# Kernel tuning notes

Hardware: AMD Instinct MI355X
Metric: run time of the kernel (lower is better)

## Reference

```python
import jax, jax.numpy as jnp
import numpy as np

B, T, D, H, O = 64, 2048, 64, 512, 128


def setup_inputs() -> dict:
    key = jax.random.key(0)
    ks = jax.random.split(key, 7)
    s = 1.0 / np.sqrt(H).astype(np.float32)  # PyTorch default uniform(-1/sqrt(H), 1/sqrt(H))
    u = lambda k, shp: jax.random.uniform(k, shp, jnp.float32, -s, s)
    return {
        "x": jax.random.normal(ks[0], (B, T, D), jnp.float32),
        "W_ih": u(ks[1], (4 * H, D)),
        "W_hh": u(ks[2], (4 * H, H)),
        "b_ih": u(ks[3], (4 * H,)),
        "b_hh": u(ks[4], (4 * H,)),
        "W_out": u(ks[5], (O, H)),
        "b_out": u(ks[6], (O,)),
        "batch_size": B,
    }


def reference(x, W_ih, W_hh, b_ih, b_hh, W_out, b_out, batch_size):
    Bv, Tv, Dv = x.shape
    Hv = W_hh.shape[1]
    # Precompute input-to-gate projections for all timesteps: [T, B, 4H]
    xg = (jnp.einsum("btd,gd->btg", x, W_ih) + b_ih + b_hh).transpose(1, 0, 2)
    h0 = jnp.zeros((Bv, Hv), x.dtype)
    c0 = jnp.zeros((Bv, Hv), x.dtype)

    def step(carry, g_t):
        h, c = carry
        g = g_t + h @ W_hh.T  # [B, 4H]
        i, f, gc, o = jnp.split(g, 4, axis=-1)  # PyTorch gate order i,f,g,o
        i = jax.nn.sigmoid(i)
        f = jax.nn.sigmoid(f)
        gc = jnp.tanh(gc)
        o = jax.nn.sigmoid(o)
        c = f * c + i * gc
        h = o * jnp.tanh(c)
        return (h, c), None

    (hT, cT), _ = jax.lax.scan(step, (h0, c0), xg)
    # Linear applied at last timestep only (module returns predictions[:, -1, :])
    pred = hT @ W_out.T + b_out  # [B, O]
    return pred, hT[None], cT[None]  # (pred, h_n[1,B,H], c_n[1,B,H])
```

## Files before the change

### kernel.cpp

```cpp
#include <hip/hip_runtime.h>
#include <hip/hip_bf16.h>


typedef short short8 __attribute__((ext_vector_type(8)));
typedef float floatx4 __attribute__((ext_vector_type(4)));

#define T_STEPS 2048
#define NBG 4
#define NGI 32
#define SB() __builtin_amdgcn_sched_barrier(0)

__device__ __forceinline__ unsigned short f2bf(float f){
    unsigned u = __builtin_bit_cast(unsigned, f);
    u += 0x7FFFu + ((u >> 16) & 1u);
    return (unsigned short)(u >> 16);
}

__device__ __forceinline__ short8 pack8(float4 a, float4 b){
    short8 s;
    s[0]=(short)f2bf(a.x); s[1]=(short)f2bf(a.y); s[2]=(short)f2bf(a.z); s[3]=(short)f2bf(a.w);
    s[4]=(short)f2bf(b.x); s[5]=(short)f2bf(b.y); s[6]=(short)f2bf(b.z); s[7]=(short)f2bf(b.w);
    return s;
}

__device__ __forceinline__ float fsigmoid(float x){ return 1.0f/(1.0f+__expf(-x)); }
__device__ __forceinline__ float ftanh(float x){ return 2.0f*fsigmoid(2.0f*x)-1.0f; }

__device__ __forceinline__ void xload4(float4* X, const float* base){
    asm volatile(
    "global_load_dwordx4 %0, %4, off\n\t"
    "global_load_dwordx4 %1, %4, off offset:16\n\t"
    "global_load_dwordx4 %2, %4, off offset:128\n\t"
    "global_load_dwordx4 %3, %4, off offset:144"
    : "=&v"(X[0]), "=&v"(X[1]), "=&v"(X[2]), "=&v"(X[3])
    : "v"(base) : "memory");
}

__device__ __forceinline__ void hload16_sc1(short8* A, const unsigned short* base){
    asm volatile(
    "global_load_dwordx4 %0, %16, off sc1\n\t"
    "global_load_dwordx4 %1, %16, off offset:64 sc1\n\t"
    "global_load_dwordx4 %2, %16, off offset:128 sc1\n\t"
    "global_load_dwordx4 %3, %16, off offset:192 sc1\n\t"
    "global_load_dwordx4 %4, %16, off offset:256 sc1\n\t"
    "global_load_dwordx4 %5, %16, off offset:320 sc1\n\t"
    "global_load_dwordx4 %6, %16, off offset:384 sc1\n\t"
    "global_load_dwordx4 %7, %16, off offset:448 sc1\n\t"
    "global_load_dwordx4 %8, %16, off offset:512 sc1\n\t"
    "global_load_dwordx4 %9, %16, off offset:576 sc1\n\t"
    "global_load_dwordx4 %10, %16, off offset:640 sc1\n\t"
    "global_load_dwordx4 %11, %16, off offset:704 sc1\n\t"
    "global_load_dwordx4 %12, %16, off offset:768 sc1\n\t"
    "global_load_dwordx4 %13, %16, off offset:832 sc1\n\t"
    "global_load_dwordx4 %14, %16, off offset:896 sc1\n\t"
    "global_load_dwordx4 %15, %16, off offset:960 sc1"
    : "=&v"(A[0]), "=&v"(A[1]), "=&v"(A[2]), "=&v"(A[3]),
      "=&v"(A[4]), "=&v"(A[5]), "=&v"(A[6]), "=&v"(A[7]),
      "=&v"(A[8]), "=&v"(A[9]), "=&v"(A[10]), "=&v"(A[11]),
      "=&v"(A[12]), "=&v"(A[13]), "=&v"(A[14]), "=&v"(A[15])
    : "v"(base) : "memory");
}

__global__ __launch_bounds__(64, 1)
void lstm_persist(const float* __restrict__ x,
                  const float* __restrict__ W_ih,
                  const float* __restrict__ W_hh,
                  const float* __restrict__ b_ih,
                  const float* __restrict__ b_hh,
                  const float* __restrict__ W_out,
                  const float* __restrict__ b_out,
                  float* __restrict__ out,
                  unsigned short* __restrict__ hbuf,
                  unsigned* __restrict__ flags)
{
    const int wg   = blockIdx.x;
    const int bg   = wg & 3;
    const int gi   = wg >> 2;
    const int lane = threadIdx.x;
    const int ln   = lane & 15;
    const int lk   = lane >> 4;
    const int hd0  = gi << 4;

    __shared__ __align__(16) unsigned short hl[256];

    short8 bw[4][18];
#pragma unroll
    for (int g = 0; g < 4; ++g){
        const int row = g * 512 + hd0 + ln;
        const float* pih = W_ih + row * 64 + lk * 8;
#pragma unroll
        for (int kk = 0; kk < 2; ++kk){
            float4 u0 = *reinterpret_cast<const float4*>(pih + kk * 32);
            float4 u1 = *reinterpret_cast<const float4*>(pih + kk * 32 + 4);
            bw[g][kk] = pack8(u0, u1);
        }
        const float* phh = W_hh + row * 512 + lk * 8;
#pragma unroll
        for (int kk = 2; kk < 18; ++kk){
            float4 u0 = *reinterpret_cast<const float4*>(phh + (kk - 2) * 32);
            float4 u1 = *reinterpret_cast<const float4*>(phh + (kk - 2) * 32 + 4);
            bw[g][kk] = pack8(u0, u1);
        }
    }

    float bias[4];
#pragma unroll
    for (int g = 0; g < 4; ++g){
        const int col = g * 512 + hd0 + ln;
        bias[g] = b_ih[col] + b_hh[col];
    }

    float c0 = 0.f, c1 = 0.f, c2 = 0.f, c3 = 0.f;
    const int xrow = bg * 16 + ln;

    const unsigned* fpoll = flags + bg * NGI + (lane & 31);
    unsigned* fme = flags + bg * NGI + gi;

    short8 a[18];
    float4 xr[4];
    xload4(xr, x + ((size_t)xrow * T_STEPS) * 64 + lk * 8);

    for (int t = 0; t < T_STEPS; ++t){
        if (t > 0){
            unsigned fv;
            do {
                asm volatile("global_load_dword %0, %1, off sc1\n\t"
                             "s_waitcnt vmcnt(0)"
                             : "=v"(fv) : "v"(fpoll) : "memory");
            } while (!__all((int)(fv >= (unsigned)t)));
            SB();
            const unsigned short* hp =
                hbuf + (size_t)((((t & 1) ^ 1) * NBG + bg) * 16 + ln) * 512 + lk * 8;
            hload16_sc1(&a[2], hp);
        } else {
            asm volatile("s_waitcnt vmcnt(0)" ::: "memory");
            SB();
        }

        a[0] = pack8(xr[0], xr[1]);
        a[1] = pack8(xr[2], xr[3]);

        floatx4 acc0 = {bias[0], bias[0], bias[0], bias[0]};
        floatx4 acc1 = {bias[1], bias[1], bias[1], bias[1]};
        floatx4 acc2 = {bias[2], bias[2], bias[2], bias[2]};
        floatx4 acc3 = {bias[3], bias[3], bias[3], bias[3]};
#pragma unroll
        for (int kk = 0; kk < 2; ++kk){
            acc0 = __builtin_amdgcn_mfma_f32_16x16x32_bf16(a[kk], bw[0][kk], acc0, 0, 0, 0);
            acc1 = __builtin_amdgcn_mfma_f32_16x16x32_bf16(a[kk], bw[1][kk], acc1, 0, 0, 0);
            acc2 = __builtin_amdgcn_mfma_f32_16x16x32_bf16(a[kk], bw[2][kk], acc2, 0, 0, 0);
            acc3 = __builtin_amdgcn_mfma_f32_16x16x32_bf16(a[kk], bw[3][kk], acc3, 0, 0, 0);
        }

        if (t > 0){
            asm volatile("s_waitcnt vmcnt(8)" ::: "memory");
            SB();
#pragma unroll
            for (int kk = 2; kk < 10; ++kk){
                acc0 = __builtin_amdgcn_mfma_f32_16x16x32_bf16(a[kk], bw[0][kk], acc0, 0, 0, 0);
                acc1 = __builtin_amdgcn_mfma_f32_16x16x32_bf16(a[kk], bw[1][kk], acc1, 0, 0, 0);
                acc2 = __builtin_amdgcn_mfma_f32_16x16x32_bf16(a[kk], bw[2][kk], acc2, 0, 0, 0);
                acc3 = __builtin_amdgcn_mfma_f32_16x16x32_bf16(a[kk], bw[3][kk], acc3, 0, 0, 0);
            }
            asm volatile("s_waitcnt vmcnt(0)" ::: "memory");
            SB();
#pragma unroll
            for (int kk = 10; kk < 18; ++kk){
                acc0 = __builtin_amdgcn_mfma_f32_16x16x32_bf16(a[kk], bw[0][kk], acc0, 0, 0, 0);
                acc1 = __builtin_amdgcn_mfma_f32_16x16x32_bf16(a[kk], bw[1][kk], acc1, 0, 0, 0);
                acc2 = __builtin_amdgcn_mfma_f32_16x16x32_bf16(a[kk], bw[2][kk], acc2, 0, 0, 0);
                acc3 = __builtin_amdgcn_mfma_f32_16x16x32_bf16(a[kk], bw[3][kk], acc3, 0, 0, 0);
            }
        }

#define EPI(R, CREG)                                                         \
        {   float iv = fsigmoid(acc0[R]);                                    \
            float fv_ = fsigmoid(acc1[R]);                                   \
            float gv = ftanh(acc2[R]);                                       \
            float ov = fsigmoid(acc3[R]);                                    \
            CREG = fv_ * CREG + iv * gv;                                     \
            float hv = ov * ftanh(CREG);                                     \
            hl[(lk * 4 + R) * 16 + ln] = f2bf(hv);                           \
            if (t == T_STEPS - 1){                                           \
                int rr = bg * 16 + lk * 4 + R;                               \
                out[8192  + rr * 512 + hd0 + ln] = hv;                       \
                out[40960 + rr * 512 + hd0 + ln] = CREG;                     \
            }                                                                \
        }
        EPI(0, c0) EPI(1, c1) EPI(2, c2) EPI(3, c3)
#undef EPI

        {
            const int tn = (t + 1 < T_STEPS) ? (t + 1) : t;
            xload4(xr, x + ((size_t)xrow * T_STEPS + (size_t)tn) * 64 + lk * 8);
        }

        asm volatile("s_waitcnt lgkmcnt(0)" ::: "memory");

        if (lane < 32){
            const int row = lane >> 1, half = lane & 1;
            short8 v = *reinterpret_cast<const short8*>(&hl[row * 16 + half * 8]);
            unsigned short* dst =
                hbuf + (size_t)(((t & 1) * NBG + bg) * 16 + row) * 512 + hd0 + half * 8;
            asm volatile("global_store_dwordx4 %0, %1, off sc1"
                         :: "v"(dst), "v"(v) : "memory");
        }
        asm volatile("s_waitcnt vmcnt(0)" ::: "memory");
        SB();
        if (lane == 0){
            unsigned one = 1u;
            asm volatile("global_atomic_add %0, %1, off sc1"
                         :: "v"(fme), "v"(one) : "memory");
        }
    }

    if (gi == 0){
        unsigned fv;
        do {
            asm volatile("global_load_dword %0, %1, off sc1\n\t"
                         "s_waitcnt vmcnt(0)"
                         : "=v"(fv) : "v"(fpoll) : "memory");
        } while (!__all((int)(fv >= (unsigned)T_STEPS)));
        SB();
        const unsigned short* hp =
            hbuf + (size_t)((1 * NBG + bg) * 16 + ln) * 512 + lk * 8;
        short8 ha[16];
        hload16_sc1(ha, hp);
        asm volatile("s_waitcnt vmcnt(0)" ::: "memory");
        SB();
#pragma unroll
        for (int o0 = 0; o0 < 8; ++o0){
            const int col = o0 * 16 + ln;
            const float* wp = W_out + col * 512 + lk * 8;
            floatx4 pa = {0.f, 0.f, 0.f, 0.f};
#pragma unroll
            for (int kk = 0; kk < 16; ++kk){
                float4 w0 = *reinterpret_cast<const float4*>(wp + kk * 32);
                float4 w1 = *reinterpret_cast<const float4*>(wp + kk * 32 + 4);
                pa = __builtin_amdgcn_mfma_f32_16x16x32_bf16(ha[kk], pack8(w0, w1), pa, 0, 0, 0);
            }
            const float bo = b_out[col];
#pragma unroll
            for (int r = 0; r < 4; ++r){
                const int rr = bg * 16 + lk * 4 + r;
                out[rr * 128 + col] = pa[r] + bo;
            }
        }
    }
}

extern "C" void kernel_launch(void* const* d_in, const int* in_sizes, int n_in,
                              void* d_out, int out_size, void* d_ws, size_t ws_size,
                              hipStream_t stream) {
    const float* x     = (const float*)d_in[0];
    const float* W_ih  = (const float*)d_in[1];
    const float* W_hh  = (const float*)d_in[2];
    const float* b_ih  = (const float*)d_in[3];
    const float* b_hh  = (const float*)d_in[4];
    const float* W_out = (const float*)d_in[5];
    const float* b_out = (const float*)d_in[6];

    const size_t HBUF_BYTES = (size_t)2 * NBG * 16 * 512 * 2;
    unsigned short* hbuf = (unsigned short*)d_ws;
    unsigned* flags = (unsigned*)((char*)d_ws + HBUF_BYTES);

    hipMemsetAsync(flags, 0, NBG * NGI * sizeof(unsigned), stream);
    lstm_persist<<<dim3(NBG * NGI), dim3(64), 0, stream>>>(
        x, W_ih, W_hh, b_ih, b_hh, W_out, b_out,
        (float*)d_out, hbuf, flags);
}
```

Measured before the change: 6.500 ms.

## Double-buffer x prefetch, pipeline flag polling, and unroll the timestep loop by two

The time loop is unrolled by two with ping-pong x registers. The next step's x load is issued right after the flag poll, so it overlaps the MFMA chain, and the vmcnt thresholds are raised to fit the extra outstanding loads. The flag spin-wait now keeps two polling loads in flight so each check does not wait for a full round-trip. This aims to cut latency on the serial per-step critical path, at the cost of more registers and redundant flag traffic.

```diff
diff --git a/kernel.cpp b/kernel.cpp
--- a/kernel.cpp
+++ b/kernel.cpp
@@ -115,63 +115,94 @@
 
     const unsigned* fpoll = flags + bg * NGI + (lane & 31);
     unsigned* fme = flags + bg * NGI + gi;
+    const unsigned one = 1u;
 
     short8 a[18];
-    float4 xr[4];
-    xload4(xr, x + ((size_t)xrow * T_STEPS) * 64 + lk * 8);
-
-    for (int t = 0; t < T_STEPS; ++t){
-        if (t > 0){
-            unsigned fv;
-            do {
-                asm volatile("global_load_dword %0, %1, off sc1\n\t"
-                             "s_waitcnt vmcnt(0)"
-                             : "=v"(fv) : "v"(fpoll) : "memory");
-            } while (!__all((int)(fv >= (unsigned)t)));
-            SB();
-            const unsigned short* hp =
-                hbuf + (size_t)((((t & 1) ^ 1) * NBG + bg) * 16 + ln) * 512 + lk * 8;
-            hload16_sc1(&a[2], hp);
-        } else {
-            asm volatile("s_waitcnt vmcnt(0)" ::: "memory");
-            SB();
-        }
-
-        a[0] = pack8(xr[0], xr[1]);
-        a[1] = pack8(xr[2], xr[3]);
-
-        floatx4 acc0 = {bias[0], bias[0], bias[0], bias[0]};
-        floatx4 acc1 = {bias[1], bias[1], bias[1], bias[1]};
-        floatx4 acc2 = {bias[2], bias[2], bias[2], bias[2]};
-        floatx4 acc3 = {bias[3], bias[3], bias[3], bias[3]};
-#pragma unroll
-        for (int kk = 0; kk < 2; ++kk){
-            acc0 = __builtin_amdgcn_mfma_f32_16x16x32_bf16(a[kk], bw[0][kk], acc0, 0, 0, 0);
-            acc1 = __builtin_amdgcn_mfma_f32_16x16x32_bf16(a[kk], bw[1][kk], acc1, 0, 0, 0);
-            acc2 = __builtin_amdgcn_mfma_f32_16x16x32_bf16(a[kk], bw[2][kk], acc2, 0, 0, 0);
-            acc3 = __builtin_amdgcn_mfma_f32_16x16x32_bf16(a[kk], bw[3][kk], acc3, 0, 0, 0);
-        }
-
-        if (t > 0){
-            asm volatile("s_waitcnt vmcnt(8)" ::: "memory");
-            SB();
-#pragma unroll
-            for (int kk = 2; kk < 10; ++kk){
-                acc0 = __builtin_amdgcn_mfma_f32_16x16x32_bf16(a[kk], bw[0][kk], acc0, 0, 0, 0);
-                acc1 = __builtin_amdgcn_mfma_f32_16x16x32_bf16(a[kk], bw[1][kk], acc1, 0, 0, 0);
-                acc2 = __builtin_amdgcn_mfma_f32_16x16x32_bf16(a[kk], bw[2][kk], acc2, 0, 0, 0);
-                acc3 = __builtin_amdgcn_mfma_f32_16x16x32_bf16(a[kk], bw[3][kk], acc3, 0, 0, 0);
-            }
-            asm volatile("s_waitcnt vmcnt(0)" ::: "memory");
-            SB();
-#pragma unroll
-            for (int kk = 10; kk < 18; ++kk){
-                acc0 = __builtin_amdgcn_mfma_f32_16x16x32_bf16(a[kk], bw[0][kk], acc0, 0, 0, 0);
-                acc1 = __builtin_amdgcn_mfma_f32_16x16x32_bf16(a[kk], bw[1][kk], acc1, 0, 0, 0);
-                acc2 = __builtin_amdgcn_mfma_f32_16x16x32_bf16(a[kk], bw[2][kk], acc2, 0, 0, 0);
-                acc3 = __builtin_amdgcn_mfma_f32_16x16x32_bf16(a[kk], bw[3][kk], acc3, 0, 0, 0);
-            }
-        }
+    float4 xrA[4], xrB[4];
+    xload4(xrA, x + ((size_t)xrow * T_STEPS) * 64 + lk * 8);
+
+#define STEP(T_, XCUR, XNXT)                                                 \
+    {                                                                        \
+        const int t = (T_);                                                  \
+        if (t > 0){                                                          \
+            unsigned fv0, fv1;                                               \
+            asm volatile("global_load_dword %0, %1, off sc1"                 \
+                         : "=v"(fv0) : "v"(fpoll) : "memory");               \
+            for (;;){                                                        \
+                asm volatile("global_load_dword %0, %1, off sc1"             \
+                             : "=v"(fv1) : "v"(fpoll) : "memory");           \
+                asm volatile("s_waitcnt vmcnt(1)" ::: "memory");             \
+                SB();                                                        \
+                if (__all((int)(fv0 >= (unsigned)t))) break;                 \
+                asm volatile("global_load_dword %0, %1, off sc1"             \
+                             : "=v"(fv0) : "v"(fpoll) : "memory");           \
+                asm volatile("s_waitcnt vmcnt(1)" ::: "memory");             \
+                SB();                                                        \
+                if (__all((int)(fv1 >= (unsigned)t))) break;                 \
+            }                                                                \
+            const unsigned short* hp =                                       \
+                hbuf + (size_t)((((t & 1) ^ 1) * NBG + bg) * 16 + ln) * 512  \
+                     + lk * 8;                                               \
+            hload16_sc1(&a[2], hp);                                          \
+        } else {                                                             \
+            asm volatile("s_waitcnt vmcnt(0)" ::: "memory");                 \
+            SB();                                                            \
+        }                                                                    \
+        {   const int tn = (t + 1 < T_STEPS) ? (t + 1) : t;                  \
+            xload4(XNXT, x + ((size_t)xrow * T_STEPS + (size_t)tn) * 64      \
+                           + lk * 8);                                        \
+        }                                                                    \
+        a[0] = pack8(XCUR[0], XCUR[1]);                                      \
+        a[1] = pack8(XCUR[2], XCUR[3]);                                      \
+        floatx4 acc0 = {bias[0], bias[0], bias[0], bias[0]};                 \
+        floatx4 acc1 = {bias[1], bias[1], bias[1], bias[1]};                 \
+        floatx4 acc2 = {bias[2], bias[2], bias[2], bias[2]};                 \
+        floatx4 acc3 = {bias[3], bias[3], bias[3], bias[3]};                 \
+        _Pragma("unroll")                                                    \
+        for (int kk = 0; kk < 2; ++kk){                                      \
+            acc0 = __builtin_amdgcn_mfma_f32_16x16x32_bf16(a[kk], bw[0][kk], acc0, 0, 0, 0); \
+            acc1 = __builtin_amdgcn_mfma_f32_16x16x32_bf16(a[kk], bw[1][kk], acc1, 0, 0, 0); \
+            acc2 = __builtin_amdgcn_mfma_f32_16x16x32_bf16(a[kk], bw[2][kk], acc2, 0, 0, 0); \
+            acc3 = __builtin_amdgcn_mfma_f32_16x16x32_bf16(a[kk], bw[3][kk], acc3, 0, 0, 0); \
+        }                                                                    \
+        if (t > 0){                                                          \
+            asm volatile("s_waitcnt vmcnt(12)" ::: "memory");                \
+            SB();                                                            \
+            _Pragma("unroll")                                                \
+            for (int kk = 2; kk < 10; ++kk){                                 \
+                acc0 = __builtin_amdgcn_mfma_f32_16x16x32_bf16(a[kk], bw[0][kk], acc0, 0, 0, 0); \
+                acc1 = __builtin_amdgcn_mfma_f32_16x16x32_bf16(a[kk], bw[1][kk], acc1, 0, 0, 0); \
+                acc2 = __builtin_amdgcn_mfma_f32_16x16x32_bf16(a[kk], bw[2][kk], acc2, 0, 0, 0); \
+                acc3 = __builtin_amdgcn_mfma_f32_16x16x32_bf16(a[kk], bw[3][kk], acc3, 0, 0, 0); \
+            }                                                                \
+            asm volatile("s_waitcnt vmcnt(4)" ::: "memory");                 \
+            SB();                                                            \
+            _Pragma("unroll")                                                \
+            for (int kk = 10; kk < 18; ++kk){                                \
+                acc0 = __builtin_amdgcn_mfma_f32_16x16x32_bf16(a[kk], bw[0][kk], acc0, 0, 0, 0); \
+                acc1 = __builtin_amdgcn_mfma_f32_16x16x32_bf16(a[kk], bw[1][kk], acc1, 0, 0, 0); \
+                acc2 = __builtin_amdgcn_mfma_f32_16x16x32_bf16(a[kk], bw[2][kk], acc2, 0, 0, 0); \
+                acc3 = __builtin_amdgcn_mfma_f32_16x16x32_bf16(a[kk], bw[3][kk], acc3, 0, 0, 0); \
+            }                                                                \
+        }                                                                    \
+        EPI(0, c0) EPI(1, c1) EPI(2, c2) EPI(3, c3)                          \
+        asm volatile("s_waitcnt lgkmcnt(0)" ::: "memory");                   \
+        if (lane < 32){                                                      \
+            const int row = lane >> 1, half = lane & 1;                      \
+            short8 v = *reinterpret_cast<const short8*>(&hl[row * 16 + half * 8]); \
+            unsigned short* dst =                                            \
+                hbuf + (size_t)(((t & 1) * NBG + bg) * 16 + row) * 512       \
+                     + hd0 + half * 8;                                       \
+            asm volatile("global_store_dwordx4 %0, %1, off sc1"              \
+                         :: "v"(dst), "v"(v) : "memory");                    \
+        }                                                                    \
+        asm volatile("s_waitcnt vmcnt(0)" ::: "memory");                     \
+        SB();                                                                \
+        if (lane == 0){                                                      \
+            asm volatile("global_atomic_add %0, %1, off sc1"                 \
+                         :: "v"(fme), "v"(one) : "memory");                  \
+        }                                                                    \
+    }
 
 #define EPI(R, CREG)                                                         \
         {   float iv = fsigmoid(acc0[R]);                                    \
@@ -187,32 +218,13 @@
                 out[40960 + rr * 512 + hd0 + ln] = CREG;                     \
             }                                                                \
         }
-        EPI(0, c0) EPI(1, c1) EPI(2, c2) EPI(3, c3)
+
+    for (int tt = 0; tt < T_STEPS; tt += 2){
+        STEP(tt,     xrA, xrB)
+        STEP(tt + 1, xrB, xrA)
+    }
+#undef STEP
 #undef EPI
-
-        {
-            const int tn = (t + 1 < T_STEPS) ? (t + 1) : t;
-            xload4(xr, x + ((size_t)xrow * T_STEPS + (size_t)tn) * 64 + lk * 8);
-        }
-
-        asm volatile("s_waitcnt lgkmcnt(0)" ::: "memory");
-
-        if (lane < 32){
-            const int row = lane >> 1, half = lane & 1;
-            short8 v = *reinterpret_cast<const short8*>(&hl[row * 16 + half * 8]);
-            unsigned short* dst =
-                hbuf + (size_t)(((t & 1) * NBG + bg) * 16 + row) * 512 + hd0 + half * 8;
-            asm volatile("global_store_dwordx4 %0, %1, off sc1"
-                         :: "v"(dst), "v"(v) : "memory");
-        }
-        asm volatile("s_waitcnt vmcnt(0)" ::: "memory");
-        SB();
-        if (lane == 0){
-            unsigned one = 1u;
-            asm volatile("global_atomic_add %0, %1, off sc1"
-                         :: "v"(fme), "v"(one) : "memory");
-        }
-    }
 
     if (gi == 0){
         unsigned fv;
```

Result: slower. 6.673 ms (+2.7%).

## Pack four gate-waves per block and share h loads through LDS

Applied to the files above, without the earlier changes.

Launches 32 blocks of 4 waves in place of 128 single-wave blocks. Each wave now loads a quarter of the previous hidden state from global memory and writes it to shared memory, and after a block barrier every wave reads the full h tile from LDS. The aim is to cut global h traffic per step by four, at the cost of an extra LDS round trip and a block-level barrier on the serial recurrence path. The epilogue's LDS staging buffer becomes per-wave.

```diff
diff --git a/kernel.cpp b/kernel.cpp
--- a/kernel.cpp
+++ b/kernel.cpp
@@ -33,6 +33,16 @@
     "global_load_dwordx4 %2, %4, off offset:128\n\t"
     "global_load_dwordx4 %3, %4, off offset:144"
     : "=&v"(X[0]), "=&v"(X[1]), "=&v"(X[2]), "=&v"(X[3])
+    : "v"(base) : "memory");
+}
+
+__device__ __forceinline__ void hload4_sc1(short8* A, const unsigned short* base){
+    asm volatile(
+    "global_load_dwordx4 %0, %4, off sc1\n\t"
+    "global_load_dwordx4 %1, %4, off offset:64 sc1\n\t"
+    "global_load_dwordx4 %2, %4, off offset:128 sc1\n\t"
+    "global_load_dwordx4 %3, %4, off offset:192 sc1"
+    : "=&v"(A[0]), "=&v"(A[1]), "=&v"(A[2]), "=&v"(A[3])
     : "v"(base) : "memory");
 }
 
@@ -61,7 +71,7 @@
     : "v"(base) : "memory");
 }
 
-__global__ __launch_bounds__(64, 1)
+__global__ __launch_bounds__(256, 1)
 void lstm_persist(const float* __restrict__ x,
                   const float* __restrict__ W_ih,
                   const float* __restrict__ W_hh,
@@ -73,15 +83,19 @@
                   unsigned short* __restrict__ hbuf,
                   unsigned* __restrict__ flags)
 {
-    const int wg   = blockIdx.x;
-    const int bg   = wg & 3;
-    const int gi   = wg >> 2;
-    const int lane = threadIdx.x;
+    const int blk  = blockIdx.x;
+    const int bg   = blk & 3;
+    const int q    = blk >> 2;
+    const int tid  = threadIdx.x;
+    const int wid  = tid >> 6;
+    const int lane = tid & 63;
     const int ln   = lane & 15;
     const int lk   = lane >> 4;
+    const int gi   = q * 4 + wid;
     const int hd0  = gi << 4;
 
-    __shared__ __align__(16) unsigned short hl[256];
+    __shared__ __align__(16) short8 hx[16][64];
+    __shared__ __align__(16) unsigned short hl[4][256];
 
     short8 bw[4][18];
 #pragma unroll
@@ -115,8 +129,10 @@
 
     const unsigned* fpoll = flags + bg * NGI + (lane & 31);
     unsigned* fme = flags + bg * NGI + gi;
+    const unsigned one = 1u;
 
     short8 a[18];
+    short8 st[4];
     float4 xr[4];
     xload4(xr, x + ((size_t)xrow * T_STEPS) * 64 + lk * 8);
 
@@ -130,8 +146,9 @@
             } while (!__all((int)(fv >= (unsigned)t)));
             SB();
             const unsigned short* hp =
-                hbuf + (size_t)((((t & 1) ^ 1) * NBG + bg) * 16 + ln) * 512 + lk * 8;
-            hload16_sc1(&a[2], hp);
+                hbuf + (size_t)((((t & 1) ^ 1) * NBG + bg) * 16 + ln) * 512
+                     + (size_t)(wid * 4) * 32 + lk * 8;
+            hload4_sc1(st, hp);
         } else {
             asm volatile("s_waitcnt vmcnt(0)" ::: "memory");
             SB();
@@ -153,23 +170,20 @@
         }
 
         if (t > 0){
-            asm volatile("s_waitcnt vmcnt(8)" ::: "memory");
-            SB();
-#pragma unroll
-            for (int kk = 2; kk < 10; ++kk){
-                acc0 = __builtin_amdgcn_mfma_f32_16x16x32_bf16(a[kk], bw[0][kk], acc0, 0, 0, 0);
-                acc1 = __builtin_amdgcn_mfma_f32_16x16x32_bf16(a[kk], bw[1][kk], acc1, 0, 0, 0);
-                acc2 = __builtin_amdgcn_mfma_f32_16x16x32_bf16(a[kk], bw[2][kk], acc2, 0, 0, 0);
-                acc3 = __builtin_amdgcn_mfma_f32_16x16x32_bf16(a[kk], bw[3][kk], acc3, 0, 0, 0);
-            }
             asm volatile("s_waitcnt vmcnt(0)" ::: "memory");
             SB();
 #pragma unroll
-            for (int kk = 10; kk < 18; ++kk){
-                acc0 = __builtin_amdgcn_mfma_f32_16x16x32_bf16(a[kk], bw[0][kk], acc0, 0, 0, 0);
-                acc1 = __builtin_amdgcn_mfma_f32_16x16x32_bf16(a[kk], bw[1][kk], acc1, 0, 0, 0);
-                acc2 = __builtin_amdgcn_mfma_f32_16x16x32_bf16(a[kk], bw[2][kk], acc2, 0, 0, 0);
-                acc3 = __builtin_amdgcn_mfma_f32_16x16x32_bf16(a[kk], bw[3][kk], acc3, 0, 0, 0);
+            for (int i = 0; i < 4; ++i)
+                hx[wid * 4 + i][lane] = st[i];
+            asm volatile("s_waitcnt lgkmcnt(0)" ::: "memory");
+            __builtin_amdgcn_s_barrier();
+#pragma unroll
+            for (int c = 0; c < 16; ++c){
+                a[c + 2] = hx[c][lane];
+                acc0 = __builtin_amdgcn_mfma_f32_16x16x32_bf16(a[c+2], bw[0][c+2], acc0, 0, 0, 0);
+                acc1 = __builtin_amdgcn_mfma_f32_16x16x32_bf16(a[c+2], bw[1][c+2], acc1, 0, 0, 0);
+                acc2 = __builtin_amdgcn_mfma_f32_16x16x32_bf16(a[c+2], bw[2][c+2], acc2, 0, 0, 0);
+                acc3 = __builtin_amdgcn_mfma_f32_16x16x32_bf16(a[c+2], bw[3][c+2], acc3, 0, 0, 0);
             }
         }
 
@@ -180,7 +194,7 @@
             float ov = fsigmoid(acc3[R]);                                    \
             CREG = fv_ * CREG + iv * gv;                                     \
             float hv = ov * ftanh(CREG);                                     \
-            hl[(lk * 4 + R) * 16 + ln] = f2bf(hv);                           \
+            hl[wid][(lk * 4 + R) * 16 + ln] = f2bf(hv);                      \
             if (t == T_STEPS - 1){                                           \
                 int rr = bg * 16 + lk * 4 + R;                               \
                 out[8192  + rr * 512 + hd0 + ln] = hv;                       \
@@ -199,7 +213,7 @@
 
         if (lane < 32){
             const int row = lane >> 1, half = lane & 1;
-            short8 v = *reinterpret_cast<const short8*>(&hl[row * 16 + half * 8]);
+            short8 v = *reinterpret_cast<const short8*>(&hl[wid][row * 16 + half * 8]);
             unsigned short* dst =
                 hbuf + (size_t)(((t & 1) * NBG + bg) * 16 + row) * 512 + hd0 + half * 8;
             asm volatile("global_store_dwordx4 %0, %1, off sc1"
@@ -208,7 +222,6 @@
         asm volatile("s_waitcnt vmcnt(0)" ::: "memory");
         SB();
         if (lane == 0){
-            unsigned one = 1u;
             asm volatile("global_atomic_add %0, %1, off sc1"
                          :: "v"(fme), "v"(one) : "memory");
         }
@@ -265,7 +278,7 @@
     unsigned* flags = (unsigned*)((char*)d_ws + HBUF_BYTES);
 
     hipMemsetAsync(flags, 0, NBG * NGI * sizeof(unsigned), stream);
-    lstm_persist<<<dim3(NBG * NGI), dim3(64), 0, stream>>>(
+    lstm_persist<<<dim3(32), dim3(256), 0, stream>>>(
         x, W_ih, W_hh, b_ih, b_hh, W_out, b_out,
         (float*)d_out, hbuf, flags);
 }
```

After: 7.844 ms. 1.21x slower.

## Replace store-wait-before-flag with in-data stamp validation of hidden state

Applied to the files above, without the earlier changes.

Each hidden-state store now embeds a 2-bit step stamp in the low mantissa bits of two bf16 elements per 16-byte chunk. The s_waitcnt between the h store and the flag atomic is removed, so the flag may become visible before the data. Consumers check the stamps after loading and reload until every chunk matches the expected step. This takes one global store round-trip off the per-step critical path, at the cost of perturbing two bf16 LSBs per chunk, possible spin reloads, and an extra memset of the h buffer.

```diff
diff --git a/kernel.cpp b/kernel.cpp
--- a/kernel.cpp
+++ b/kernel.cpp
@@ -115,12 +115,17 @@
 
     const unsigned* fpoll = flags + bg * NGI + (lane & 31);
     unsigned* fme = flags + bg * NGI + gi;
+    const unsigned one = 1u;
 
     short8 a[18];
+    short8 stv = {0,0,0,0,0,0,0,0};
     float4 xr[4];
     xload4(xr, x + ((size_t)xrow * T_STEPS) * 64 + lk * 8);
 
     for (int t = 0; t < T_STEPS; ++t){
+        const unsigned short* hp =
+            hbuf + (size_t)((((t & 1) ^ 1) * NBG + bg) * 16 + ln) * 512 + lk * 8;
+
         if (t > 0){
             unsigned fv;
             do {
@@ -129,12 +134,12 @@
                              : "=v"(fv) : "v"(fpoll) : "memory");
             } while (!__all((int)(fv >= (unsigned)t)));
             SB();
-            const unsigned short* hp =
-                hbuf + (size_t)((((t & 1) ^ 1) * NBG + bg) * 16 + ln) * 512 + lk * 8;
+            asm volatile("" :: "v"(stv));
             hload16_sc1(&a[2], hp);
         } else {
             asm volatile("s_waitcnt vmcnt(0)" ::: "memory");
             SB();
+            asm volatile("" :: "v"(stv));
         }
 
         a[0] = pack8(xr[0], xr[1]);
@@ -153,19 +158,24 @@
         }
 
         if (t > 0){
-            asm volatile("s_waitcnt vmcnt(8)" ::: "memory");
-            SB();
-#pragma unroll
-            for (int kk = 2; kk < 10; ++kk){
-                acc0 = __builtin_amdgcn_mfma_f32_16x16x32_bf16(a[kk], bw[0][kk], acc0, 0, 0, 0);
-                acc1 = __builtin_amdgcn_mfma_f32_16x16x32_bf16(a[kk], bw[1][kk], acc1, 0, 0, 0);
-                acc2 = __builtin_amdgcn_mfma_f32_16x16x32_bf16(a[kk], bw[2][kk], acc2, 0, 0, 0);
-                acc3 = __builtin_amdgcn_mfma_f32_16x16x32_bf16(a[kk], bw[3][kk], acc3, 0, 0, 0);
-            }
             asm volatile("s_waitcnt vmcnt(0)" ::: "memory");
             SB();
-#pragma unroll
-            for (int kk = 10; kk < 18; ++kk){
+            const unsigned expst = (((unsigned)(t - 1) >> 1) & 1u) + 1u;
+            for (;;){
+                int ok = 1;
+#pragma unroll
+                for (int c = 2; c < 18; ++c){
+                    unsigned s = ((unsigned)(unsigned short)a[c][6] & 1u)
+                               | (((unsigned)(unsigned short)a[c][7] & 1u) << 1);
+                    ok &= (s == expst) ? 1 : 0;
+                }
+                if (__all(ok)) break;
+                hload16_sc1(&a[2], hp);
+                asm volatile("s_waitcnt vmcnt(0)" ::: "memory");
+                SB();
+            }
+#pragma unroll
+            for (int kk = 2; kk < 18; ++kk){
                 acc0 = __builtin_amdgcn_mfma_f32_16x16x32_bf16(a[kk], bw[0][kk], acc0, 0, 0, 0);
                 acc1 = __builtin_amdgcn_mfma_f32_16x16x32_bf16(a[kk], bw[1][kk], acc1, 0, 0, 0);
                 acc2 = __builtin_amdgcn_mfma_f32_16x16x32_bf16(a[kk], bw[2][kk], acc2, 0, 0, 0);
@@ -197,20 +207,23 @@
 
         asm volatile("s_waitcnt lgkmcnt(0)" ::: "memory");
 
-        if (lane < 32){
-            const int row = lane >> 1, half = lane & 1;
-            short8 v = *reinterpret_cast<const short8*>(&hl[row * 16 + half * 8]);
-            unsigned short* dst =
-                hbuf + (size_t)(((t & 1) * NBG + bg) * 16 + row) * 512 + hd0 + half * 8;
-            asm volatile("global_store_dwordx4 %0, %1, off sc1"
-                         :: "v"(dst), "v"(v) : "memory");
-        }
-        asm volatile("s_waitcnt vmcnt(0)" ::: "memory");
-        SB();
-        if (lane == 0){
-            unsigned one = 1u;
-            asm volatile("global_atomic_add %0, %1, off sc1"
-                         :: "v"(fme), "v"(one) : "memory");
+        {
+            const unsigned stamp = (((unsigned)t >> 1) & 1u) + 1u;
+            if (lane < 32){
+                const int row = lane >> 1, half = lane & 1;
+                short8 v = *reinterpret_cast<const short8*>(&hl[row * 16 + half * 8]);
+                v[6] = (short)((v[6] & ~(short)1) | (short)(stamp & 1u));
+                v[7] = (short)((v[7] & ~(short)1) | (short)((stamp >> 1) & 1u));
+                stv = v;
+                unsigned short* dst =
+                    hbuf + (size_t)(((t & 1) * NBG + bg) * 16 + row) * 512 + hd0 + half * 8;
+                asm volatile("global_store_dwordx4 %0, %1, off sc1"
+                             :: "v"(dst), "v"(stv) : "memory");
+            }
+            if (lane == 0){
+                asm volatile("global_atomic_add %0, %1, off sc1"
+                             :: "v"(fme), "v"(one) : "memory");
+            }
         }
     }
 
@@ -222,11 +235,23 @@
                          : "=v"(fv) : "v"(fpoll) : "memory");
         } while (!__all((int)(fv >= (unsigned)T_STEPS)));
         SB();
+        const unsigned expst = (((unsigned)(T_STEPS - 1) >> 1) & 1u) + 1u;
         const unsigned short* hp =
             hbuf + (size_t)((1 * NBG + bg) * 16 + ln) * 512 + lk * 8;
         short8 ha[16];
-        hload16_sc1(ha, hp);
-        asm volatile("s_waitcnt vmcnt(0)" ::: "memory");
+        int ok;
+        do {
+            hload16_sc1(ha, hp);
+            asm volatile("s_waitcnt vmcnt(0)" ::: "memory");
+            SB();
+            ok = 1;
+#pragma unroll
+            for (int kk = 0; kk < 16; ++kk){
+                unsigned s = ((unsigned)(unsigned short)ha[kk][6] & 1u)
+                           | (((unsigned)(unsigned short)ha[kk][7] & 1u) << 1);
+                ok &= (s == expst) ? 1 : 0;
+            }
+        } while (!__all(ok));
         SB();
 #pragma unroll
         for (int o0 = 0; o0 < 8; ++o0){
@@ -264,6 +289,7 @@
     unsigned short* hbuf = (unsigned short*)d_ws;
     unsigned* flags = (unsigned*)((char*)d_ws + HBUF_BYTES);
 
+    hipMemsetAsync(hbuf, 0, HBUF_BYTES, stream);
     hipMemsetAsync(flags, 0, NBG * NGI * sizeof(unsigned), stream);
     lstm_persist<<<dim3(NBG * NGI), dim3(64), 0, stream>>>(
         x, W_ih, W_hh, b_ih, b_hh, W_out, b_out,
```

Measured after the change: 6.783 ms. 4.4% more time.
